# Optimization experiments

Hardware: AMD Instinct MI355X
Metric: run time of the kernel (lower is better)

Reference implementation:

```python
import jax, jax.numpy as jnp
import numpy as np

USER_NUM = 50000
ITEM_NUM = 50000
N = USER_NUM + ITEM_NUM
VT_DIM = 512
CAT_NUM = 1000
CAT_DIM = 32
HIDDEN = 128
OUT = 64
E = 2_000_000
BAG = 5


def setup_inputs() -> dict:
    key = jax.random.key(0)
    ks = jax.random.split(key, 12)
    inp = {
        "vt_feature": jax.random.normal(ks[0], (ITEM_NUM, VT_DIM), jnp.float32),
        "cat_indices": jax.random.randint(ks[1], (ITEM_NUM * BAG,), 0, CAT_NUM),
        "cat_offsets": jnp.arange(ITEM_NUM) * BAG,
        "edge_index": jax.random.randint(ks[2], (2, E), 0, N),
        # learned parameters
        "cat_table": jax.random.normal(ks[3], (CAT_NUM, CAT_DIM), jnp.float32) * 0.1,
        "fuse_w": jax.random.normal(ks[4], (HIDDEN, VT_DIM + CAT_DIM), jnp.float32) * (1.0 / np.sqrt(VT_DIM + CAT_DIM)),
        "user": jax.random.normal(ks[5], (USER_NUM, HIDDEN), jnp.float32) * 0.1,
        "w1_l": jax.random.normal(ks[6], (HIDDEN, HIDDEN), jnp.float32) * (1.0 / np.sqrt(HIDDEN)),
        "b1": jnp.zeros((HIDDEN,), jnp.float32),
        "w1_r": jax.random.normal(ks[7], (HIDDEN, HIDDEN), jnp.float32) * (1.0 / np.sqrt(HIDDEN)),
        "w2_l": jax.random.normal(ks[8], (OUT, HIDDEN), jnp.float32) * (1.0 / np.sqrt(HIDDEN)),
        "b2": jnp.zeros((OUT,), jnp.float32),
        "w2_r": jax.random.normal(ks[9], (OUT, HIDDEN), jnp.float32) * (1.0 / np.sqrt(HIDDEN)),
    }
    return inp


def _embedding_bag_mean(table, indices, offsets, num_bags):
    # EmbeddingBag(mode='mean') with offsets: segment-mean of table lookups.
    pos = jnp.arange(indices.shape[0])
    seg = jnp.searchsorted(offsets, pos, side="right") - 1  # bag id per index
    sums = jax.ops.segment_sum(table[indices], seg, num_segments=num_bags)
    cnt = jax.ops.segment_sum(jnp.ones_like(pos, jnp.float32), seg, num_segments=num_bags)
    return sums / jnp.maximum(cnt, 1.0)[:, None]


def _sage_conv(x, edge_index, w_l, b_l, w_r):
    # PyG SAGEConv (aggr='mean'): lin_l(mean_{j->i} x_j) + lin_r(x_i)
    src, dst = edge_index[0], edge_index[1]
    agg = jax.ops.segment_sum(x[src], dst, num_segments=N)
    deg = jax.ops.segment_sum(jnp.ones((src.shape[0],), x.dtype), dst, num_segments=N)
    agg = agg / jnp.maximum(deg, 1.0)[:, None]
    return agg @ w_l.T + b_l + x @ w_r.T


def reference(vt_feature, cat_indices, cat_offsets, edge_index, cat_table,
              fuse_w, user, w1_l, b1, w1_r, w2_l, b2, w2_r):
    cat_emb = _embedding_bag_mean(cat_table, cat_indices, cat_offsets, ITEM_NUM)
    item_feat = jnp.concatenate([vt_feature, cat_emb], axis=1) @ fuse_w.T
    x0 = jnp.concatenate([user, item_feat], axis=0)  # [N, hidden]
    x1 = jax.nn.leaky_relu(_sage_conv(x0, edge_index, w1_l, b1, w1_r), negative_slope=0.01)
    # dropout is identity in eval mode
    x2 = _sage_conv(x1, edge_index, w2_l, b2, w2_r)
    return x2
```

## Files before the change

### kernel.cpp

```cpp
#include <hip/hip_runtime.h>

#define USER_N   50000
#define ITEM_N   50000
#define NNODE    100000
#define VT_DIM   512
#define CAT_DIM  32
#define HIDDEN   128
#define OUTD     64
#define PADCAP   64

#define BINC    8192
#define NBKT    98
#define BSHIFT  10
#define SLICES  8
#define BKT_CAP 24576

#define AGG_BLOCKS 4096

typedef __attribute__((ext_vector_type(8))) short short8;
typedef __attribute__((ext_vector_type(4))) float f32x4;

__device__ __forceinline__ float bf2f(unsigned short u) {
    return __uint_as_float(((unsigned int)u) << 16);
}
__device__ __forceinline__ unsigned short f2bf(float f) {
    unsigned int u = __float_as_uint(f);
    unsigned int r = u + 0x7fffu + ((u >> 16) & 1u);
    return (unsigned short)(r >> 16);
}
__device__ __forceinline__ unsigned int pk2(float lo, float hi) {
    return ((unsigned int)f2bf(hi) << 16) | (unsigned int)f2bf(lo);
}
__device__ __forceinline__ short8 cvt8(float4 a, float4 b) {
    union { unsigned short u[8]; short8 s; } r;
    r.u[0] = f2bf(a.x); r.u[1] = f2bf(a.y); r.u[2] = f2bf(a.z); r.u[3] = f2bf(a.w);
    r.u[4] = f2bf(b.x); r.u[5] = f2bf(b.y); r.u[6] = f2bf(b.z); r.u[7] = f2bf(b.w);
    return r.s;
}
__device__ __forceinline__ void acc8w(float* a, uint4 v, float w) {
    a[0] += w * __uint_as_float(v.x << 16);
    a[1] += w * __uint_as_float(v.x & 0xffff0000u);
    a[2] += w * __uint_as_float(v.y << 16);
    a[3] += w * __uint_as_float(v.y & 0xffff0000u);
    a[4] += w * __uint_as_float(v.z << 16);
    a[5] += w * __uint_as_float(v.z & 0xffff0000u);
    a[6] += w * __uint_as_float(v.w << 16);
    a[7] += w * __uint_as_float(v.w & 0xffff0000u);
}

__global__ __launch_bounds__(256) void k_copy_user(const float* __restrict__ user,
                                                   unsigned short* __restrict__ x0, int n4) {
    int gid = blockIdx.x * 256 + threadIdx.x;
    if (gid >= n4) return;
    float4 v = ((const float4*)user)[gid];
    ushort4 o;
    o.x = f2bf(v.x); o.y = f2bf(v.y); o.z = f2bf(v.z); o.w = f2bf(v.w);
    ((ushort4*)x0)[gid] = o;
}

#define ASTR 40
#define XSTR 136
#define BSTR 552

__global__ __launch_bounds__(1024, 1) void k_fuse_mfma(const float* __restrict__ vt,
                                                       const float* __restrict__ cat_table,
                                                       const int* __restrict__ cat_idx,
                                                       const int* __restrict__ cat_off,
                                                       const float* __restrict__ fw,
                                                       unsigned short* __restrict__ x0,
                                                       int total_idx) {
    __shared__ __align__(16) unsigned short Bl[128 * BSTR];
    int tid = threadIdx.x;

#pragma unroll
    for (int i = 0; i < 17; i++) {
        int idx = tid + i * 1024;
        int col = idx / 136;
        int k4 = idx - col * 136;
        float4 v = *(const float4*)(fw + (size_t)col * (VT_DIM + CAT_DIM) + k4 * 4);
        ushort4 o;
        o.x = f2bf(v.x); o.y = f2bf(v.y); o.z = f2bf(v.z); o.w = f2bf(v.w);
        *(ushort4*)&Bl[col * BSTR + k4 * 4] = o;
    }
    __syncthreads();

    int wave = tid >> 6, lane = tid & 63, quad = lane >> 4, l16 = lane & 15;
    int t = blockIdx.x + (wave << 8);
    if (t >= (ITEM_N + 15) / 16) return;
    int r0 = t * 16;

    short8 cav;
    {
        int item = r0 + l16;
        int s = cat_off[item];
        int e = (item + 1 < ITEM_N) ? cat_off[item + 1] : total_idx;
        float a[8];
#pragma unroll
        for (int i = 0; i < 8; i++) a[i] = 0.f;
        for (int j = s; j < e; ++j) {
            const float* cr = cat_table + (size_t)cat_idx[j] * CAT_DIM + quad * 8;
            float4 c0 = ((const float4*)cr)[0];
            float4 c1 = ((const float4*)cr)[1];
            a[0] += c0.x; a[1] += c0.y; a[2] += c0.z; a[3] += c0.w;
            a[4] += c1.x; a[5] += c1.y; a[6] += c1.z; a[7] += c1.w;
        }
        int cnt = e - s;
        float inv = 1.f / (float)(cnt > 0 ? cnt : 1);
        float4 f0 = {a[0] * inv, a[1] * inv, a[2] * inv, a[3] * inv};
        float4 f1 = {a[4] * inv, a[5] * inv, a[6] * inv, a[7] * inv};
        cav = cvt8(f0, f1);
    }

    f32x4 acc[8];
#pragma unroll
    for (int n = 0; n < 8; n++) acc[n] = (f32x4){0.f, 0.f, 0.f, 0.f};

    const float* vrow = vt + (size_t)(r0 + l16) * VT_DIM + quad * 8;
    for (int kb = 0; kb < 17; ++kb) {
        short8 av;
        if (kb < 16) {
            float4 v0 = *(const float4*)(vrow + kb * 32);
            float4 v1 = *(const float4*)(vrow + kb * 32 + 4);
            av = cvt8(v0, v1);
        } else {
            av = cav;
        }
#pragma unroll
        for (int nf = 0; nf < 8; nf++) {
            short8 bv = *(const short8*)&Bl[(nf * 16 + l16) * BSTR + kb * 32 + quad * 8];
            acc[nf] = __builtin_amdgcn_mfma_f32_16x16x32_bf16(av, bv, acc[nf], 0, 0, 0);
        }
    }

    int rbase = r0 + quad * 4;
#pragma unroll
    for (int r = 0; r < 4; r++) {
        int orow = rbase + r;
        if (orow < ITEM_N) {
#pragma unroll
            for (int nf = 0; nf < 8; nf++) {
                int col = nf * 16 + l16;
                x0[(size_t)(USER_N + orow) * HIDDEN + col] = f2bf(acc[nf][r]);
            }
        }
    }
}

__global__ __launch_bounds__(256, 4) void k_l12_mfma(const unsigned short* __restrict__ agg1,
                                                     const unsigned short* __restrict__ x0,
                                                     const float* __restrict__ w1l,
                                                     const float* __restrict__ w1r,
                                                     const float* __restrict__ b1,
                                                     const float* __restrict__ w2l,
                                                     const float* __restrict__ w2r,
                                                     const float* __restrict__ b2,
                                                     unsigned short* __restrict__ y1,
                                                     float* __restrict__ outw) {
    __shared__ __align__(16) unsigned short Al[64 * ASTR];
    __shared__ __align__(16) unsigned short Bl[128 * ASTR];
    __shared__ __align__(16) unsigned short Xl[64 * XSTR];
    int tid = threadIdx.x;
    int wave = tid >> 6, lane = tid & 63, quad = lane >> 4, l16 = lane & 15;
    int br0 = blockIdx.x * 64;
    int row = tid >> 2, q4 = tid & 3;
    int arow = br0 + row;

    f32x4 acc[8];
#pragma unroll
    for (int n = 0; n < 8; n++) acc[n] = (f32x4){0.f, 0.f, 0.f, 0.f};

    for (int kb = 0; kb < 8; ++kb) {
        const unsigned short* abase = (kb < 4) ? agg1 : x0;
        int kc = (kb & 3) * 32;
        if (arow < NNODE) {
            uint4 v = *(const uint4*)(abase + (size_t)arow * HIDDEN + kc + q4 * 8);
            *(uint4*)&Al[row * ASTR + q4 * 8] = v;
        } else {
            uint4 z = {0, 0, 0, 0};
            *(uint4*)&Al[row * ASTR + q4 * 8] = z;
        }
        {
            int n = tid & 127, kh = tid >> 7;
            const float* src = ((kb < 4) ? w1l : w1r) + (size_t)n * HIDDEN + kc + kh * 16;
#pragma unroll
            for (int i = 0; i < 4; i++) {
                float4 v = ((const float4*)src)[i];
                ushort4 o;
                o.x = f2bf(v.x); o.y = f2bf(v.y); o.z = f2bf(v.z); o.w = f2bf(v.w);
                *(ushort4*)&Bl[n * ASTR + kh * 16 + i * 4] = o;
            }
        }
        __syncthreads();
        short8 av = *(const short8*)&Al[(wave * 16 + l16) * ASTR + quad * 8];
#pragma unroll
        for (int nf = 0; nf < 8; nf++) {
            short8 bv = *(const short8*)&Bl[(nf * 16 + l16) * ASTR + quad * 8];
            acc[nf] = __builtin_amdgcn_mfma_f32_16x16x32_bf16(av, bv, acc[nf], 0, 0, 0);
        }
        __syncthreads();
    }
    {
        float bias[8];
#pragma unroll
        for (int nf = 0; nf < 8; nf++) bias[nf] = b1[nf * 16 + l16];
        int lr0 = wave * 16 + quad * 4;
#pragma unroll
        for (int r = 0; r < 4; r++) {
#pragma unroll
            for (int nf = 0; nf < 8; nf++) {
                float v = acc[nf][r] + bias[nf];
                v = (v >= 0.f) ? v : 0.01f * v;
                Xl[(lr0 + r) * XSTR + nf * 16 + l16] = f2bf(v);
            }
        }
    }
    __syncthreads();

#pragma unroll
    for (int n = 0; n < 8; n++) acc[n] = (f32x4){0.f, 0.f, 0.f, 0.f};
    for (int kb = 0; kb < 4; ++kb) {
        int kc = kb * 32;
        {
            int n = tid & 127, kh = tid >> 7;
            const float* wsrc = (n < 64) ? (w2l + (size_t)n * HIDDEN)
                                         : (w2r + (size_t)(n - 64) * HIDDEN);
            const float* src = wsrc + kc + kh * 16;
#pragma unroll
            for (int i = 0; i < 4; i++) {
                float4 v = ((const float4*)src)[i];
                ushort4 o;
                o.x = f2bf(v.x); o.y = f2bf(v.y); o.z = f2bf(v.z); o.w = f2bf(v.w);
                *(ushort4*)&Bl[n * ASTR + kh * 16 + i * 4] = o;
            }
        }
        __syncthreads();
        short8 av = *(const short8*)&Xl[(wave * 16 + l16) * XSTR + kc + quad * 8];
#pragma unroll
        for (int nf = 0; nf < 8; nf++) {
            short8 bv = *(const short8*)&Bl[(nf * 16 + l16) * ASTR + quad * 8];
            acc[nf] = __builtin_amdgcn_mfma_f32_16x16x32_bf16(av, bv, acc[nf], 0, 0, 0);
        }
        __syncthreads();
    }
    float bias2[4];
#pragma unroll
    for (int nf = 0; nf < 4; nf++) bias2[nf] = b2[nf * 16 + l16];
    int rbase = br0 + wave * 16 + quad * 4;
#pragma unroll
    for (int r = 0; r < 4; r++) {
        int orow = rbase + r;
        if (orow < NNODE) {
#pragma unroll
            for (int nf = 0; nf < 4; nf++) {
                int col = nf * 16 + l16;
                y1[(size_t)orow * OUTD + col] = f2bf(acc[nf][r]);
            }
#pragma unroll
            for (int nf = 4; nf < 8; nf++) {
                int col = (nf - 4) * 16 + l16;
                outw[(size_t)orow * OUTD + col] = acc[nf][r] + bias2[nf - 4];
            }
        }
    }
}

__global__ __launch_bounds__(256) void k_deg(const int* __restrict__ dst, int ne4, int ne, int* __restrict__ deg) {
    int t = blockIdx.x * 256 + threadIdx.x;
    int base = t * 4;
    if (t < ne4) {
        int4 d4 = *(const int4*)&dst[base];
        atomicAdd(&deg[d4.x], 1);
        atomicAdd(&deg[d4.y], 1);
        atomicAdd(&deg[d4.z], 1);
        atomicAdd(&deg[d4.w], 1);
    } else {
        for (int e = base; e < ne; ++e) atomicAdd(&deg[dst[e]], 1);
    }
}

__global__ __launch_bounds__(256) void k_scanA(const int* __restrict__ deg, int n, int* __restrict__ bsum) {
    __shared__ int sd[256];
    int i = blockIdx.x * 256 + threadIdx.x;
    sd[threadIdx.x] = (i < n) ? deg[i] : 0;
    __syncthreads();
    for (int o = 128; o > 0; o >>= 1) {
        if (threadIdx.x < o) sd[threadIdx.x] += sd[threadIdx.x + o];
        __syncthreads();
    }
    if (threadIdx.x == 0) bsum[blockIdx.x] = sd[0];
}

__global__ __launch_bounds__(512) void k_scanB(const int* __restrict__ bsum, int nb, int* __restrict__ boff) {
    __shared__ int sd[512];
    int t = threadIdx.x;
    int v = (t < nb) ? bsum[t] : 0;
    sd[t] = v;
    __syncthreads();
    for (int o = 1; o < 512; o <<= 1) {
        int x = 0;
        if (t >= o) x = sd[t - o];
        __syncthreads();
        sd[t] += x;
        __syncthreads();
    }
    if (t < nb) boff[t] = sd[t] - v;
}

__global__ __launch_bounds__(256) void k_scanC(const int* __restrict__ deg, int n,
                                               const int* __restrict__ boff,
                                               int* __restrict__ offs, int* __restrict__ cursor, int ne) {
    __shared__ int sd[256];
    int i = blockIdx.x * 256 + threadIdx.x;
    int v = (i < n) ? deg[i] : 0;
    sd[threadIdx.x] = v;
    __syncthreads();
    for (int o = 1; o < 256; o <<= 1) {
        int x = 0;
        if (threadIdx.x >= o) x = sd[threadIdx.x - o];
        __syncthreads();
        sd[threadIdx.x] += x;
        __syncthreads();
    }
    if (i < n) {
        int ex = boff[blockIdx.x] + sd[threadIdx.x] - v;
        offs[i] = ex;
        cursor[i] = ex;
    }
    if (i == 0) offs[n] = ne;
}

__global__ __launch_bounds__(256) void k_scatter(const int* __restrict__ src, const int* __restrict__ dst,
                                                 int ne4, int ne, int* __restrict__ cursor, int* __restrict__ csr) {
    int t = blockIdx.x * 256 + threadIdx.x;
    int base = t * 4;
    if (t < ne4) {
        int4 d4 = *(const int4*)&dst[base];
        int4 s4 = *(const int4*)&src[base];
        int p0 = atomicAdd(&cursor[d4.x], 1);
        int p1 = atomicAdd(&cursor[d4.y], 1);
        int p2 = atomicAdd(&cursor[d4.z], 1);
        int p3 = atomicAdd(&cursor[d4.w], 1);
        csr[p0] = s4.x;
        csr[p1] = s4.y;
        csr[p2] = s4.z;
        csr[p3] = s4.w;
    } else {
        for (int e = base; e < ne; ++e) {
            int slot = atomicAdd(&cursor[dst[e]], 1);
            csr[slot] = src[e];
        }
    }
}

__global__ __launch_bounds__(256) void k_binscatter_f(const int* __restrict__ src,
                                                      const int* __restrict__ dst,
                                                      int ne,
                                                      int* __restrict__ bktcnt,
                                                      int2* __restrict__ ebin) {
    __shared__ int lh[NBKT];
    int b = blockIdx.x;
    for (int i = threadIdx.x; i < NBKT; i += 256) lh[i] = 0;
    __syncthreads();
    int s = b * BINC;
    int e = (s + BINC < ne) ? (s + BINC) : ne;
    int nv = (e - s) & ~3;
    for (int j = s + threadIdx.x * 4; j < s + nv; j += 1024) {
        int4 d4 = *(const int4*)&dst[j];
        atomicAdd(&lh[d4.x >> BSHIFT], 1);
        atomicAdd(&lh[d4.y >> BSHIFT], 1);
        atomicAdd(&lh[d4.z >> BSHIFT], 1);
        atomicAdd(&lh[d4.w >> BSHIFT], 1);
    }
    for (int j = s + nv + threadIdx.x; j < e; j += 256) {
        atomicAdd(&lh[dst[j] >> BSHIFT], 1);
    }
    __syncthreads();
    for (int i = threadIdx.x; i < NBKT; i += 256) lh[i] = atomicAdd(&bktcnt[i], lh[i]);
    __syncthreads();
    for (int j = s + threadIdx.x * 4; j < s + nv; j += 1024) {
        int4 d4 = *(const int4*)&dst[j];
        int4 s4 = *(const int4*)&src[j];
        int b0 = d4.x >> BSHIFT, b1_ = d4.y >> BSHIFT, b2_ = d4.z >> BSHIFT, b3 = d4.w >> BSHIFT;
        int p0 = atomicAdd(&lh[b0], 1);
        int p1 = atomicAdd(&lh[b1_], 1);
        int p2 = atomicAdd(&lh[b2_], 1);
        int p3 = atomicAdd(&lh[b3], 1);
        if (p0 < BKT_CAP) ebin[(size_t)b0 * BKT_CAP + p0] = make_int2(s4.x, d4.x);
        if (p1 < BKT_CAP) ebin[(size_t)b1_ * BKT_CAP + p1] = make_int2(s4.y, d4.y);
        if (p2 < BKT_CAP) ebin[(size_t)b2_ * BKT_CAP + p2] = make_int2(s4.z, d4.z);
        if (p3 < BKT_CAP) ebin[(size_t)b3 * BKT_CAP + p3] = make_int2(s4.w, d4.w);
    }
    for (int j = s + nv + threadIdx.x; j < e; j += 256) {
        int d = dst[j];
        int b0 = d >> BSHIFT;
        int p = atomicAdd(&lh[b0], 1);
        if (p < BKT_CAP) ebin[(size_t)b0 * BKT_CAP + p] = make_int2(src[j], d);
    }
}

__global__ __launch_bounds__(256) void k_scatter_bkt(const int2* __restrict__ ebin,
                                                     const int* __restrict__ bktcnt,
                                                     int* __restrict__ cursor,
                                                     int* __restrict__ csrp) {
    int xcd = blockIdx.x & 7;
    int w = blockIdx.x >> 3;
    int i = w / SLICES, sl = w - i * SLICES;
    int b = xcd + (i << 3);
    if (b >= NBKT) return;
    int len = bktcnt[b];
    if (len > BKT_CAP) len = BKT_CAP;
    int s0 = b * BKT_CAP;
    int e0 = s0 + len;
    int per = (len + SLICES - 1) / SLICES;
    int s = s0 + sl * per;
    int e = (s + per < e0) ? (s + per) : e0;
    for (int j = s + threadIdx.x; j < e; j += 256) {
        int2 p = ebin[j];
        int slot = atomicAdd(&cursor[p.y], 1);
        if (slot < PADCAP) csrp[p.y * PADCAP + slot] = p.x;
    }
}

__global__ __launch_bounds__(256) void k_agg1(const unsigned short* __restrict__ x0,
                                              const int* __restrict__ offs,
                                              const int* __restrict__ cnts,
                                              int pad,
                                              const int* __restrict__ csr,
                                              unsigned short* __restrict__ agg1) {
    int lane = threadIdx.x & 63;
    int quad = lane >> 4;
    int l16 = lane & 15;
    int wstride = gridDim.x << 2;
    for (int wid = (blockIdx.x << 2) + (threadIdx.x >> 6); wid < NNODE; wid += wstride) {
        int s, e, d;
        if (pad) {
            s = wid << 6;
            int c = cnts[wid];
            d = c;
            e = s + (c < PADCAP ? c : PADCAP);
        } else {
            s = offs[wid];
            e = offs[wid + 1];
            d = e - s;
        }
        float a[8];
#pragma unroll
        for (int i = 0; i < 8; i++) a[i] = 0.f;
        for (int j = s; j < e; j += 32) {
            int sn[8];
            float w[8];
#pragma unroll
            for (int t = 0; t < 8; t++) {
                int myj = j + 4 * t + quad;
                bool ok = (myj < e);
                sn[t] = ok ? csr[myj] : csr[s];
                w[t] = ok ? 1.f : 0.f;
            }
            uint4 v[8];
#pragma unroll
            for (int t = 0; t < 8; t++)
                v[t] = *(const uint4*)&x0[(size_t)sn[t] * HIDDEN + l16 * 8];
#pragma unroll
            for (int t = 0; t < 8; t++) acc8w(a, v[t], w[t]);
        }
#pragma unroll
        for (int i = 0; i < 8; i++) {
            a[i] += __shfl_xor(a[i], 16, 64);
            a[i] += __shfl_xor(a[i], 32, 64);
        }
        float inv = 1.f / (float)(d > 0 ? d : 1);
        if (quad == 0) {
            uint4 o;
            o.x = pk2(a[0] * inv, a[1] * inv);
            o.y = pk2(a[2] * inv, a[3] * inv);
            o.z = pk2(a[4] * inv, a[5] * inv);
            o.w = pk2(a[6] * inv, a[7] * inv);
            *(uint4*)&agg1[(size_t)wid * HIDDEN + l16 * 8] = o;
        }
    }
}

__global__ __launch_bounds__(256) void k_agg2_out(const unsigned short* __restrict__ y1,
                                                  const int* __restrict__ offs,
                                                  const int* __restrict__ cnts,
                                                  int pad,
                                                  const int* __restrict__ csr,
                                                  float* __restrict__ out) {
    int lane = threadIdx.x & 63;
    int oct = lane >> 3;
    int l8 = lane & 7;
    int wstride = gridDim.x << 2;
    for (int wid = (blockIdx.x << 2) + (threadIdx.x >> 6); wid < NNODE; wid += wstride) {
        int s, e, d;
        if (pad) {
            s = wid << 6;
            int c = cnts[wid];
            d = c;
            e = s + (c < PADCAP ? c : PADCAP);
        } else {
            s = offs[wid];
            e = offs[wid + 1];
            d = e - s;
        }
        float a[8];
#pragma unroll
        for (int i = 0; i < 8; i++) a[i] = 0.f;
        for (int j = s; j < e; j += 64) {
            int sn[8];
            float w[8];
#pragma unroll
            for (int t = 0; t < 8; t++) {
                int myj = j + 8 * t + oct;
                bool ok = (myj < e);
                sn[t] = ok ? csr[myj] : csr[s];
                w[t] = ok ? 1.f : 0.f;
            }
            uint4 v[8];
#pragma unroll
            for (int t = 0; t < 8; t++)
                v[t] = *(const uint4*)&y1[(size_t)sn[t] * OUTD + l8 * 8];
#pragma unroll
            for (int t = 0; t < 8; t++) acc8w(a, v[t], w[t]);
        }
#pragma unroll
        for (int i = 0; i < 8; i++) {
            a[i] += __shfl_xor(a[i], 8, 64);
            a[i] += __shfl_xor(a[i], 16, 64);
            a[i] += __shfl_xor(a[i], 32, 64);
        }
        float inv = 1.f / (float)(d > 0 ? d : 1);
        if (oct == 0) {
            float4* op = (float4*)&out[(size_t)wid * OUTD + l8 * 8];
            float4 p0 = op[0];
            float4 p1 = op[1];
            float4 o0, o1;
            o0.x = a[0] * inv + p0.x; o0.y = a[1] * inv + p0.y;
            o0.z = a[2] * inv + p0.z; o0.w = a[3] * inv + p0.w;
            o1.x = a[4] * inv + p1.x; o1.y = a[5] * inv + p1.y;
            o1.z = a[6] * inv + p1.z; o1.w = a[7] * inv + p1.w;
            op[0] = o0;
            op[1] = o1;
        }
    }
}

extern "C" void kernel_launch(void* const* d_in, const int* in_sizes, int n_in,
                              void* d_out, int out_size, void* d_ws, size_t ws_size,
                              hipStream_t stream) {
    const float* vt      = (const float*)d_in[0];
    const int*   cat_idx = (const int*)d_in[1];
    const int*   cat_off = (const int*)d_in[2];
    const int*   ei      = (const int*)d_in[3];
    const float* cat_tab = (const float*)d_in[4];
    const float* fuse_w  = (const float*)d_in[5];
    const float* user    = (const float*)d_in[6];
    const float* w1l     = (const float*)d_in[7];
    const float* b1      = (const float*)d_in[8];
    const float* w1r     = (const float*)d_in[9];
    const float* w2l     = (const float*)d_in[10];
    const float* b2      = (const float*)d_in[11];
    const float* w2r     = (const float*)d_in[12];
    float* out = (float*)d_out;

    const int ne = in_sizes[3] / 2;
    const int ne4 = ne / 4;
    const int total_idx = in_sizes[1];
    const int* esrc = ei;
    const int* edst = ei + ne;

    const size_t SZ_X0  = (size_t)NNODE * HIDDEN * 2;
    const size_t SZ_PAD = (size_t)NNODE * PADCAP * 4;
    const size_t SZ_CSR = (size_t)ne * 4;
    const size_t SZ_INT = (size_t)NNODE * 4;
    const size_t SZ_EBIN = (size_t)NBKT * BKT_CAP * 8;

    size_t need_pad = SZ_X0 * 2 + (SZ_EBIN > SZ_X0 ? SZ_EBIN : SZ_X0) + SZ_PAD + SZ_INT + 8192;
    size_t need_csr = SZ_X0 * 3 + SZ_CSR + SZ_INT * 3 + 4 * 4096 + 4096;

    char* p = (char*)d_ws;
    auto alloc = [&](size_t bytes) {
        char* q = p;
        p += (bytes + 255) & ~(size_t)255;
        return q;
    };

    const int nscan = (NNODE + 255) / 256;
    const int sc_blocks = (ne4 + 255) / 256;
    const int nblk = (ne + BINC - 1) / BINC;

    if (ws_size >= need_pad) {
        unsigned short* x0   = (unsigned short*)alloc(SZ_X0);
        unsigned short* aggY = (unsigned short*)alloc(SZ_X0);
        char*           SCR  = (char*)alloc(SZ_EBIN > SZ_X0 ? SZ_EBIN : SZ_X0);
        int*            csrp = (int*)alloc(SZ_PAD);
        int*          cursor = (int*)alloc(SZ_INT + 1024);
        int*          bktcnt = cursor + NNODE;

        int2*           ebin = (int2*)SCR;
        unsigned short* y1   = (unsigned short*)SCR;

        k_copy_user<<<(USER_N * HIDDEN / 4 + 255) / 256, 256, 0, stream>>>(user, x0, USER_N * HIDDEN / 4);
        k_fuse_mfma<<<256, 1024, 0, stream>>>(vt, cat_tab, cat_idx, cat_off, fuse_w, x0, total_idx);

        hipMemsetAsync(cursor, 0, SZ_INT + 1024, stream);
        k_binscatter_f<<<nblk, 256, 0, stream>>>(esrc, edst, ne, bktcnt, ebin);
        k_scatter_bkt<<<8 * 13 * SLICES, 256, 0, stream>>>(ebin, bktcnt, cursor, csrp);

        k_agg1<<<AGG_BLOCKS, 256, 0, stream>>>(x0, cursor, cursor, 1, csrp, aggY);
        k_l12_mfma<<<(NNODE + 63) / 64, 256, 0, stream>>>(aggY, x0, w1l, w1r, b1, w2l, w2r, b2, y1, out);
        k_agg2_out<<<AGG_BLOCKS, 256, 0, stream>>>(y1, cursor, cursor, 1, csrp, out);
    } else if (ws_size >= need_csr) {
        unsigned short* x0   = (unsigned short*)alloc(SZ_X0);
        unsigned short* aggY = (unsigned short*)alloc(SZ_X0);
        unsigned short* y1   = (unsigned short*)alloc(SZ_X0);
        char*           R4   = (char*)alloc(SZ_CSR);
        int* deg    = (int*)alloc(SZ_INT);
        int* offs   = (int*)alloc(SZ_INT + 256);
        int* cursor = (int*)alloc(SZ_INT);
        int* bsum   = (int*)alloc(512 * 4);
        int* boff   = (int*)alloc(512 * 4);
        int* csr    = (int*)R4;

        k_copy_user<<<(USER_N * HIDDEN / 4 + 255) / 256, 256, 0, stream>>>(user, x0, USER_N * HIDDEN / 4);
        k_fuse_mfma<<<256, 1024, 0, stream>>>(vt, cat_tab, cat_idx, cat_off, fuse_w, x0, total_idx);

        hipMemsetAsync(deg, 0, SZ_INT, stream);
        k_deg<<<sc_blocks, 256, 0, stream>>>(edst, ne4, ne, deg);
        k_scanA<<<nscan, 256, 0, stream>>>(deg, NNODE, bsum);
        k_scanB<<<1, 512, 0, stream>>>(bsum, nscan, boff);
        k_scanC<<<nscan, 256, 0, stream>>>(deg, NNODE, boff, offs, cursor, ne);
        k_scatter<<<sc_blocks, 256, 0, stream>>>(esrc, edst, ne4, ne, cursor, csr);

        k_agg1<<<AGG_BLOCKS, 256, 0, stream>>>(x0, offs, offs, 0, csr, aggY);
        k_l12_mfma<<<(NNODE + 63) / 64, 256, 0, stream>>>(aggY, x0, w1l, w1r, b1, w2l, w2r, b2, y1, out);
        k_agg2_out<<<AGG_BLOCKS, 256, 0, stream>>>(y1, offs, offs, 0, csr, out);
    } else {
        hipMemsetAsync(d_out, 0, (size_t)out_size * 4, stream);
    }
}
```

Baseline: 470.3 us.

## Make layer GEMM kernel persistent with LDS-resident weights; fold user copy into fuse

```diff
diff --git a/kernel.cpp b/kernel.cpp
--- a/kernel.cpp
+++ b/kernel.cpp
@@ -58,15 +58,17 @@
     ((ushort4*)x0)[gid] = o;
 }
 
-#define ASTR 40
-#define XSTR 136
 #define BSTR 552
+#define W1STR 264
+#define W2STR 132
+#define XWSTR 132
 
 __global__ __launch_bounds__(1024, 1) void k_fuse_mfma(const float* __restrict__ vt,
                                                        const float* __restrict__ cat_table,
                                                        const int* __restrict__ cat_idx,
                                                        const int* __restrict__ cat_off,
                                                        const float* __restrict__ fw,
+                                                       const float* __restrict__ user,
                                                        unsigned short* __restrict__ x0,
                                                        int total_idx) {
     __shared__ __align__(16) unsigned short Bl[128 * BSTR];
@@ -86,57 +88,56 @@
 
     int wave = tid >> 6, lane = tid & 63, quad = lane >> 4, l16 = lane & 15;
     int t = blockIdx.x + (wave << 8);
-    if (t >= (ITEM_N + 15) / 16) return;
-    int r0 = t * 16;
-
-    short8 cav;
-    {
-        int item = r0 + l16;
-        int s = cat_off[item];
-        int e = (item + 1 < ITEM_N) ? cat_off[item + 1] : total_idx;
-        float a[8];
-#pragma unroll
-        for (int i = 0; i < 8; i++) a[i] = 0.f;
-        for (int j = s; j < e; ++j) {
-            const float* cr = cat_table + (size_t)cat_idx[j] * CAT_DIM + quad * 8;
-            float4 c0 = ((const float4*)cr)[0];
-            float4 c1 = ((const float4*)cr)[1];
-            a[0] += c0.x; a[1] += c0.y; a[2] += c0.z; a[3] += c0.w;
-            a[4] += c1.x; a[5] += c1.y; a[6] += c1.z; a[7] += c1.w;
-        }
-        int cnt = e - s;
-        float inv = 1.f / (float)(cnt > 0 ? cnt : 1);
-        float4 f0 = {a[0] * inv, a[1] * inv, a[2] * inv, a[3] * inv};
-        float4 f1 = {a[4] * inv, a[5] * inv, a[6] * inv, a[7] * inv};
-        cav = cvt8(f0, f1);
-    }
-
-    f32x4 acc[8];
-#pragma unroll
-    for (int n = 0; n < 8; n++) acc[n] = (f32x4){0.f, 0.f, 0.f, 0.f};
-
-    const float* vrow = vt + (size_t)(r0 + l16) * VT_DIM + quad * 8;
-    for (int kb = 0; kb < 17; ++kb) {
-        short8 av;
-        if (kb < 16) {
-            float4 v0 = *(const float4*)(vrow + kb * 32);
-            float4 v1 = *(const float4*)(vrow + kb * 32 + 4);
-            av = cvt8(v0, v1);
-        } else {
-            av = cav;
-        }
-#pragma unroll
-        for (int nf = 0; nf < 8; nf++) {
-            short8 bv = *(const short8*)&Bl[(nf * 16 + l16) * BSTR + kb * 32 + quad * 8];
-            acc[nf] = __builtin_amdgcn_mfma_f32_16x16x32_bf16(av, bv, acc[nf], 0, 0, 0);
-        }
-    }
-
-    int rbase = r0 + quad * 4;
-#pragma unroll
-    for (int r = 0; r < 4; r++) {
-        int orow = rbase + r;
-        if (orow < ITEM_N) {
+    if (t < (ITEM_N + 15) / 16) {
+        int r0 = t * 16;
+
+        short8 cav;
+        {
+            int item = r0 + l16;
+            int s = cat_off[item];
+            int e = (item + 1 < ITEM_N) ? cat_off[item + 1] : total_idx;
+            float a[8];
+#pragma unroll
+            for (int i = 0; i < 8; i++) a[i] = 0.f;
+            for (int j = s; j < e; ++j) {
+                const float* cr = cat_table + (size_t)cat_idx[j] * CAT_DIM + quad * 8;
+                float4 c0 = ((const float4*)cr)[0];
+                float4 c1 = ((const float4*)cr)[1];
+                a[0] += c0.x; a[1] += c0.y; a[2] += c0.z; a[3] += c0.w;
+                a[4] += c1.x; a[5] += c1.y; a[6] += c1.z; a[7] += c1.w;
+            }
+            int cnt = e - s;
+            float inv = 1.f / (float)(cnt > 0 ? cnt : 1);
+            float4 f0 = {a[0] * inv, a[1] * inv, a[2] * inv, a[3] * inv};
+            float4 f1 = {a[4] * inv, a[5] * inv, a[6] * inv, a[7] * inv};
+            cav = cvt8(f0, f1);
+        }
+
+        f32x4 acc[8];
+#pragma unroll
+        for (int n = 0; n < 8; n++) acc[n] = (f32x4){0.f, 0.f, 0.f, 0.f};
+
+        const float* vrow = vt + (size_t)(r0 + l16) * VT_DIM + quad * 8;
+        for (int kb = 0; kb < 17; ++kb) {
+            short8 av;
+            if (kb < 16) {
+                float4 v0 = *(const float4*)(vrow + kb * 32);
+                float4 v1 = *(const float4*)(vrow + kb * 32 + 4);
+                av = cvt8(v0, v1);
+            } else {
+                av = cav;
+            }
+#pragma unroll
+            for (int nf = 0; nf < 8; nf++) {
+                short8 bv = *(const short8*)&Bl[(nf * 16 + l16) * BSTR + kb * 32 + quad * 8];
+                acc[nf] = __builtin_amdgcn_mfma_f32_16x16x32_bf16(av, bv, acc[nf], 0, 0, 0);
+            }
+        }
+
+        int rbase = r0 + quad * 4;
+#pragma unroll
+        for (int r = 0; r < 4; r++) {
+            int orow = rbase + r;
 #pragma unroll
             for (int nf = 0; nf < 8; nf++) {
                 int col = nf * 16 + l16;
@@ -144,9 +145,16 @@
             }
         }
     }
-}
-
-__global__ __launch_bounds__(256, 4) void k_l12_mfma(const unsigned short* __restrict__ agg1,
+
+    for (int g = blockIdx.x * 1024 + tid; g < USER_N * HIDDEN / 4; g += 256 * 1024) {
+        float4 v = ((const float4*)user)[g];
+        ushort4 o;
+        o.x = f2bf(v.x); o.y = f2bf(v.y); o.z = f2bf(v.z); o.w = f2bf(v.w);
+        ((ushort4*)x0)[g] = o;
+    }
+}
+
+__global__ __launch_bounds__(768, 1) void k_l12_mfma(const unsigned short* __restrict__ agg1,
                                                      const unsigned short* __restrict__ x0,
                                                      const float* __restrict__ w1l,
                                                      const float* __restrict__ w1r,
@@ -156,110 +164,91 @@
                                                      const float* __restrict__ b2,
                                                      unsigned short* __restrict__ y1,
                                                      float* __restrict__ outw) {
-    __shared__ __align__(16) unsigned short Al[64 * ASTR];
-    __shared__ __align__(16) unsigned short Bl[128 * ASTR];
-    __shared__ __align__(16) unsigned short Xl[64 * XSTR];
+    __shared__ __align__(16) unsigned short Wl1[128 * W1STR];
+    __shared__ __align__(16) unsigned short Wl2[128 * W2STR];
+    __shared__ __align__(16) unsigned short Xw[12 * 16 * XWSTR];
     int tid = threadIdx.x;
+
+    for (int idx = tid; idx < 4096; idx += 768) {
+        int o = idx >> 5, k4 = idx & 31;
+        float4 v = *(const float4*)(w1l + (size_t)o * HIDDEN + k4 * 4);
+        ushort4 q;
+        q.x = f2bf(v.x); q.y = f2bf(v.y); q.z = f2bf(v.z); q.w = f2bf(v.w);
+        *(ushort4*)&Wl1[o * W1STR + k4 * 4] = q;
+        v = *(const float4*)(w1r + (size_t)o * HIDDEN + k4 * 4);
+        q.x = f2bf(v.x); q.y = f2bf(v.y); q.z = f2bf(v.z); q.w = f2bf(v.w);
+        *(ushort4*)&Wl1[o * W1STR + 128 + k4 * 4] = q;
+    }
+    for (int idx = tid; idx < 2048; idx += 768) {
+        int o = idx >> 5, k4 = idx & 31;
+        float4 v = *(const float4*)(w2l + (size_t)o * HIDDEN + k4 * 4);
+        ushort4 q;
+        q.x = f2bf(v.x); q.y = f2bf(v.y); q.z = f2bf(v.z); q.w = f2bf(v.w);
+        *(ushort4*)&Wl2[o * W2STR + k4 * 4] = q;
+        v = *(const float4*)(w2r + (size_t)o * HIDDEN + k4 * 4);
+        q.x = f2bf(v.x); q.y = f2bf(v.y); q.z = f2bf(v.z); q.w = f2bf(v.w);
+        *(ushort4*)&Wl2[(o + 64) * W2STR + k4 * 4] = q;
+    }
+    __syncthreads();
+
     int wave = tid >> 6, lane = tid & 63, quad = lane >> 4, l16 = lane & 15;
-    int br0 = blockIdx.x * 64;
-    int row = tid >> 2, q4 = tid & 3;
-    int arow = br0 + row;
-
-    f32x4 acc[8];
-#pragma unroll
-    for (int n = 0; n < 8; n++) acc[n] = (f32x4){0.f, 0.f, 0.f, 0.f};
-
-    for (int kb = 0; kb < 8; ++kb) {
-        const unsigned short* abase = (kb < 4) ? agg1 : x0;
-        int kc = (kb & 3) * 32;
-        if (arow < NNODE) {
-            uint4 v = *(const uint4*)(abase + (size_t)arow * HIDDEN + kc + q4 * 8);
-            *(uint4*)&Al[row * ASTR + q4 * 8] = v;
-        } else {
-            uint4 z = {0, 0, 0, 0};
-            *(uint4*)&Al[row * ASTR + q4 * 8] = z;
-        }
-        {
-            int n = tid & 127, kh = tid >> 7;
-            const float* src = ((kb < 4) ? w1l : w1r) + (size_t)n * HIDDEN + kc + kh * 16;
-#pragma unroll
-            for (int i = 0; i < 4; i++) {
-                float4 v = ((const float4*)src)[i];
-                ushort4 o;
-                o.x = f2bf(v.x); o.y = f2bf(v.y); o.z = f2bf(v.z); o.w = f2bf(v.w);
-                *(ushort4*)&Bl[n * ASTR + kh * 16 + i * 4] = o;
-            }
-        }
-        __syncthreads();
-        short8 av = *(const short8*)&Al[(wave * 16 + l16) * ASTR + quad * 8];
-#pragma unroll
-        for (int nf = 0; nf < 8; nf++) {
-            short8 bv = *(const short8*)&Bl[(nf * 16 + l16) * ASTR + quad * 8];
-            acc[nf] = __builtin_amdgcn_mfma_f32_16x16x32_bf16(av, bv, acc[nf], 0, 0, 0);
-        }
-        __syncthreads();
-    }
-    {
-        float bias[8];
-#pragma unroll
-        for (int nf = 0; nf < 8; nf++) bias[nf] = b1[nf * 16 + l16];
-        int lr0 = wave * 16 + quad * 4;
+    unsigned short* Xl = &Xw[wave * 16 * XWSTR];
+    float bias1[8];
+#pragma unroll
+    for (int nf = 0; nf < 8; nf++) bias1[nf] = b1[nf * 16 + l16];
+    float bias2[4];
+#pragma unroll
+    for (int nf = 0; nf < 4; nf++) bias2[nf] = b2[nf * 16 + l16];
+
+    for (int t = blockIdx.x * 12 + wave; t < NNODE / 16; t += 256 * 12) {
+        int r0 = t * 16;
+        const unsigned short* ar = agg1 + (size_t)(r0 + l16) * HIDDEN + quad * 8;
+        const unsigned short* xr = x0 + (size_t)(r0 + l16) * HIDDEN + quad * 8;
+
+        f32x4 acc[8];
+#pragma unroll
+        for (int n = 0; n < 8; n++) acc[n] = (f32x4){0.f, 0.f, 0.f, 0.f};
+#pragma unroll
+        for (int kb = 0; kb < 8; ++kb) {
+            short8 av = (kb < 4) ? *(const short8*)(ar + (kb & 3) * 32)
+                                 : *(const short8*)(xr + (kb & 3) * 32);
+#pragma unroll
+            for (int nf = 0; nf < 8; nf++) {
+                short8 bv = *(const short8*)&Wl1[(nf * 16 + l16) * W1STR + kb * 32 + quad * 8];
+                acc[nf] = __builtin_amdgcn_mfma_f32_16x16x32_bf16(av, bv, acc[nf], 0, 0, 0);
+            }
+        }
 #pragma unroll
         for (int r = 0; r < 4; r++) {
 #pragma unroll
             for (int nf = 0; nf < 8; nf++) {
-                float v = acc[nf][r] + bias[nf];
+                float v = acc[nf][r] + bias1[nf];
                 v = (v >= 0.f) ? v : 0.01f * v;
-                Xl[(lr0 + r) * XSTR + nf * 16 + l16] = f2bf(v);
-            }
-        }
-    }
-    __syncthreads();
-
-#pragma unroll
-    for (int n = 0; n < 8; n++) acc[n] = (f32x4){0.f, 0.f, 0.f, 0.f};
-    for (int kb = 0; kb < 4; ++kb) {
-        int kc = kb * 32;
-        {
-            int n = tid & 127, kh = tid >> 7;
-            const float* wsrc = (n < 64) ? (w2l + (size_t)n * HIDDEN)
-                                         : (w2r + (size_t)(n - 64) * HIDDEN);
-            const float* src = wsrc + kc + kh * 16;
-#pragma unroll
-            for (int i = 0; i < 4; i++) {
-                float4 v = ((const float4*)src)[i];
-                ushort4 o;
-                o.x = f2bf(v.x); o.y = f2bf(v.y); o.z = f2bf(v.z); o.w = f2bf(v.w);
-                *(ushort4*)&Bl[n * ASTR + kh * 16 + i * 4] = o;
-            }
-        }
-        __syncthreads();
-        short8 av = *(const short8*)&Xl[(wave * 16 + l16) * XSTR + kc + quad * 8];
-#pragma unroll
-        for (int nf = 0; nf < 8; nf++) {
-            short8 bv = *(const short8*)&Bl[(nf * 16 + l16) * ASTR + quad * 8];
-            acc[nf] = __builtin_amdgcn_mfma_f32_16x16x32_bf16(av, bv, acc[nf], 0, 0, 0);
-        }
-        __syncthreads();
-    }
-    float bias2[4];
-#pragma unroll
-    for (int nf = 0; nf < 4; nf++) bias2[nf] = b2[nf * 16 + l16];
-    int rbase = br0 + wave * 16 + quad * 4;
-#pragma unroll
-    for (int r = 0; r < 4; r++) {
-        int orow = rbase + r;
-        if (orow < NNODE) {
-#pragma unroll
-            for (int nf = 0; nf < 4; nf++) {
-                int col = nf * 16 + l16;
-                y1[(size_t)orow * OUTD + col] = f2bf(acc[nf][r]);
-            }
-#pragma unroll
-            for (int nf = 4; nf < 8; nf++) {
-                int col = (nf - 4) * 16 + l16;
-                outw[(size_t)orow * OUTD + col] = acc[nf][r] + bias2[nf - 4];
-            }
+                Xl[(quad * 4 + r) * XWSTR + nf * 16 + l16] = f2bf(v);
+            }
+        }
+        f32x4 acc2[8];
+#pragma unroll
+        for (int n = 0; n < 8; n++) acc2[n] = (f32x4){0.f, 0.f, 0.f, 0.f};
+#pragma unroll
+        for (int kb = 0; kb < 4; ++kb) {
+            short8 av = *(const short8*)&Xl[l16 * XWSTR + kb * 32 + quad * 8];
+#pragma unroll
+            for (int nf = 0; nf < 8; nf++) {
+                short8 bv = *(const short8*)&Wl2[(nf * 16 + l16) * W2STR + kb * 32 + quad * 8];
+                acc2[nf] = __builtin_amdgcn_mfma_f32_16x16x32_bf16(av, bv, acc2[nf], 0, 0, 0);
+            }
+        }
+        int rb = r0 + quad * 4;
+#pragma unroll
+        for (int r = 0; r < 4; r++) {
+            int orow = rb + r;
+#pragma unroll
+            for (int nf = 0; nf < 4; nf++)
+                y1[(size_t)orow * OUTD + nf * 16 + l16] = f2bf(acc2[nf][r]);
+#pragma unroll
+            for (int nf = 4; nf < 8; nf++)
+                outw[(size_t)orow * OUTD + (nf - 4) * 16 + l16] = acc2[nf][r] + bias2[nf - 4];
         }
     }
 }
@@ -599,15 +588,15 @@
         int2*           ebin = (int2*)SCR;
         unsigned short* y1   = (unsigned short*)SCR;
 
-        k_copy_user<<<(USER_N * HIDDEN / 4 + 255) / 256, 256, 0, stream>>>(user, x0, USER_N * HIDDEN / 4);
-        k_fuse_mfma<<<256, 1024, 0, stream>>>(vt, cat_tab, cat_idx, cat_off, fuse_w, x0, total_idx);
-
         hipMemsetAsync(cursor, 0, SZ_INT + 1024, stream);
+
+        k_fuse_mfma<<<256, 1024, 0, stream>>>(vt, cat_tab, cat_idx, cat_off, fuse_w, user, x0, total_idx);
+
         k_binscatter_f<<<nblk, 256, 0, stream>>>(esrc, edst, ne, bktcnt, ebin);
         k_scatter_bkt<<<8 * 13 * SLICES, 256, 0, stream>>>(ebin, bktcnt, cursor, csrp);
 
         k_agg1<<<AGG_BLOCKS, 256, 0, stream>>>(x0, cursor, cursor, 1, csrp, aggY);
-        k_l12_mfma<<<(NNODE + 63) / 64, 256, 0, stream>>>(aggY, x0, w1l, w1r, b1, w2l, w2r, b2, y1, out);
+        k_l12_mfma<<<256, 768, 0, stream>>>(aggY, x0, w1l, w1r, b1, w2l, w2r, b2, y1, out);
         k_agg2_out<<<AGG_BLOCKS, 256, 0, stream>>>(y1, cursor, cursor, 1, csrp, out);
     } else if (ws_size >= need_csr) {
         unsigned short* x0   = (unsigned short*)alloc(SZ_X0);
@@ -621,10 +610,10 @@
         int* boff   = (int*)alloc(512 * 4);
         int* csr    = (int*)R4;
 
-        k_copy_user<<<(USER_N * HIDDEN / 4 + 255) / 256, 256, 0, stream>>>(user, x0, USER_N * HIDDEN / 4);
-        k_fuse_mfma<<<256, 1024, 0, stream>>>(vt, cat_tab, cat_idx, cat_off, fuse_w, x0, total_idx);
-
         hipMemsetAsync(deg, 0, SZ_INT, stream);
+
+        k_fuse_mfma<<<256, 1024, 0, stream>>>(vt, cat_tab, cat_idx, cat_off, fuse_w, user, x0, total_idx);
+
         k_deg<<<sc_blocks, 256, 0, stream>>>(edst, ne4, ne, deg);
         k_scanA<<<nscan, 256, 0, stream>>>(deg, NNODE, bsum);
         k_scanB<<<1, 512, 0, stream>>>(bsum, nscan, boff);
@@ -632,7 +621,7 @@
         k_scatter<<<sc_blocks, 256, 0, stream>>>(esrc, edst, ne4, ne, cursor, csr);
 
         k_agg1<<<AGG_BLOCKS, 256, 0, stream>>>(x0, offs, offs, 0, csr, aggY);
-        k_l12_mfma<<<(NNODE + 63) / 64, 256, 0, stream>>>(aggY, x0, w1l, w1r, b1, w2l, w2r, b2, y1, out);
+        k_l12_mfma<<<256, 768, 0, stream>>>(aggY, x0, w1l, w1r, b1, w2l, w2r, b2, y1, out);
         k_agg2_out<<<AGG_BLOCKS, 256, 0, stream>>>(y1, offs, offs, 0, csr, out);
     } else {
         hipMemsetAsync(d_out, 0, (size_t)out_size * 4, stream);
```

Result: slower. 636.4 us (+35.3%).
